# Kernel optimization log

Hardware: AMD Instinct MI355X
Metric: run time of the kernel (lower is better)

Reference implementation:

```python
import jax, jax.numpy as jnp
import numpy as np

B, T, I, H = 8192, 2048, 2, 20


def setup_inputs() -> dict:
    key = jax.random.key(0)
    ks = jax.random.split(key, 7)
    s = 1.0 / np.sqrt(H).astype(np.float32)  # PyTorch RNN/Linear init bound
    u = lambda k, shp: jax.random.uniform(k, shp, minval=-s, maxval=s, dtype=jnp.float32)
    return {
        "x": jax.random.normal(ks[0], (B, T, I), dtype=jnp.float32),
        "W_ih": u(ks[1], (H, I)),
        "W_hh": u(ks[2], (H, H)),
        "b_ih": u(ks[3], (H,)),
        "b_hh": u(ks[4], (H,)),
        "fc_w": u(ks[5], (1, H)),
        "fc_b": u(ks[6], (1,)),
    }


def reference(x, W_ih, W_hh, b_ih, b_hh, fc_w, fc_b):
    # x: [B, T, I] (batch_first). Precompute input contribution for all steps.
    # xw: [T, B, H] -- time-major for lax.scan
    xw = jnp.einsum("bti,hi->tbh", x, W_ih) + b_ih + b_hh
    h0 = jnp.zeros((x.shape[0], H), dtype=x.dtype)

    def step(h, xw_t):
        h_new = jnp.tanh(xw_t + h @ W_hh.T)  # tanh-RNN recurrence
        return h_new, None

    hT, _ = jax.lax.scan(step, h0, xw)
    out = hT @ fc_w.T + fc_b          # fc on last timestep: [B, 1]
    h_state = hT[None]                # [1, B, H] like nn.RNN's h_n
    return out, h_state
```

## Files before the change

### kernel.cpp

```cpp
#include <hip/hip_runtime.h>


#define T_STEPS 2048
#define B_ROWS  8192
#define NCHUNK  (T_STEPS / 8)

#define XOR1_CTRL 0xB1
#define XOR2_CTRL 0x4E
#define MIR7_CTRL 0x141

#define ROW_F 28

typedef float f32x2 __attribute__((ext_vector_type(2)));

__device__ __forceinline__ float tanh_fast(float a) {
    float e = __builtin_amdgcn_exp2f(a * 2.8853900817779268f);
    float r = __builtin_amdgcn_rcpf(e + 1.0f);
    return fmaf(-2.0f, r, 1.0f);
}

template <int CTRL>
__device__ __forceinline__ float dpp_full(float v) {
    return __int_as_float(__builtin_amdgcn_update_dpp(
        0, __float_as_int(v), CTRL, 0xF, 0xF, true));
}

__device__ __forceinline__ void pk_fma_acc(f32x2& c, f32x2 a, f32x2 b) {
    asm("v_pk_fma_f32 %0, %1, %2, %0" : "+v"(c) : "v"(a), "v"(b));
}
__device__ __forceinline__ f32x2 pk_fma3(f32x2 a, f32x2 b, f32x2 c) {
    f32x2 d;
    asm("v_pk_fma_f32 %0, %1, %2, %3" : "=v"(d) : "v"(a), "v"(b), "v"(c));
    return d;
}

__global__ __launch_bounds__(64, 1) void rnn_fused(
    const float* __restrict__ x,
    const float* __restrict__ W_ih,
    const float* __restrict__ W_hh,
    const float* __restrict__ b_ih,
    const float* __restrict__ b_hh,
    const float* __restrict__ fc_w,
    const float* __restrict__ fc_b,
    float* __restrict__ out)
{
    const int lane = threadIdx.x & 63;
    const int g    = lane & 7;
    const int r    = lane >> 3;
    const int row  = blockIdx.x * 8 + r;

    __shared__ float hsm[8 * ROW_F];

    f32x2 W2[3][12];
    f32x2 wiP[3], bP[3];
    float fcw[3];
#pragma unroll
    for (int jj = 0; jj < 3; ++jj) {
        const int j = 3 * g + jj;
        const bool v = (j < 20);
#pragma unroll
        for (int p = 0; p < 12; ++p) {
            const int k0 = 2 * p, k1 = 2 * p + 1;
            W2[jj][p].x = (v && k0 < 20) ? W_hh[j * 20 + k0] : 0.0f;
            W2[jj][p].y = (v && k1 < 20) ? W_hh[j * 20 + k1] : 0.0f;
        }
        wiP[jj].x = v ? W_ih[j * 2 + 0] : 0.0f;
        wiP[jj].y = v ? W_ih[j * 2 + 1] : 0.0f;
        bP[jj].x  = v ? (b_ih[j] + b_hh[j]) : 0.0f;
        bP[jj].y  = 0.0f;
        fcw[jj]   = v ? fc_w[j] : 0.0f;
    }

    float*       hw   = &hsm[r * ROW_F + 3 * g];
    const float4* hr4 = (const float4*)&hsm[r * ROW_F];

    float h0 = 0.0f, h1 = 0.0f, h2 = 0.0f;
    float4 hq[6];

    hw[0] = 0.0f; hw[1] = 0.0f; hw[2] = 0.0f;
#pragma unroll
    for (int i = 0; i < 6; ++i) hq[i] = hr4[i];

    auto step = [&](float x0, float x1) {
        f32x2 xp; xp.x = x0; xp.y = x1;
        f32x2 c0 = pk_fma3(xp, wiP[0], bP[0]);
        f32x2 c1 = pk_fma3(xp, wiP[1], bP[1]);
        f32x2 c2 = pk_fma3(xp, wiP[2], bP[2]);
        const f32x2* hp = (const f32x2*)hq;
#pragma unroll
        for (int p = 0; p < 12; ++p) {
            pk_fma_acc(c0, hp[p], W2[0][p]);
            pk_fma_acc(c1, hp[p], W2[1][p]);
            pk_fma_acc(c2, hp[p], W2[2][p]);
        }
        h0 = tanh_fast(c0.x + c0.y);
        h1 = tanh_fast(c1.x + c1.y);
        h2 = tanh_fast(c2.x + c2.y);
        hw[0] = h0; hw[1] = h1; hw[2] = h2;
#pragma unroll
        for (int i = 0; i < 6; ++i) hq[i] = hr4[i];
    };

    const float4* xq = (const float4*)(x + (size_t)row * (T_STEPS * 2));
    float4 q[4], qn[4];
#pragma unroll
    for (int i = 0; i < 4; ++i) q[i] = xq[i];

#pragma unroll 1
    for (int c = 0; c < NCHUNK; c += 2) {
        const int c1 = c + 1;
        const int c2 = (c + 2 < NCHUNK) ? (c + 2) : c1;
#pragma unroll
        for (int i = 0; i < 4; ++i) qn[i] = xq[4 * c1 + i];

        step(q[0].x, q[0].y); step(q[0].z, q[0].w);
        step(q[1].x, q[1].y); step(q[1].z, q[1].w);
        step(q[2].x, q[2].y); step(q[2].z, q[2].w);
        step(q[3].x, q[3].y); step(q[3].z, q[3].w);

#pragma unroll
        for (int i = 0; i < 4; ++i) q[i] = xq[4 * c2 + i];

        step(qn[0].x, qn[0].y); step(qn[0].z, qn[0].w);
        step(qn[1].x, qn[1].y); step(qn[1].z, qn[1].w);
        step(qn[2].x, qn[2].y); step(qn[2].z, qn[2].w);
        step(qn[3].x, qn[3].y); step(qn[3].z, qn[3].w);
    }

    {
        const int j0 = 3 * g;
        float* hs = out + B_ROWS + (size_t)row * 20;
        if (j0 + 0 < 20) hs[j0 + 0] = h0;
        if (j0 + 1 < 20) hs[j0 + 1] = h1;
        if (j0 + 2 < 20) hs[j0 + 2] = h2;
    }
    {
        float p = h0 * fcw[0];
        p = fmaf(h1, fcw[1], p);
        p = fmaf(h2, fcw[2], p);
        p += dpp_full<XOR1_CTRL>(p);
        p += dpp_full<XOR2_CTRL>(p);
        p += dpp_full<MIR7_CTRL>(p);
        if (g == 0) out[row] = p + fc_b[0];
    }
}

extern "C" void kernel_launch(void* const* d_in, const int* in_sizes, int n_in,
                              void* d_out, int out_size, void* d_ws, size_t ws_size,
                              hipStream_t stream) {
    const float* x    = (const float*)d_in[0];
    const float* W_ih = (const float*)d_in[1];
    const float* W_hh = (const float*)d_in[2];
    const float* b_ih = (const float*)d_in[3];
    const float* b_hh = (const float*)d_in[4];
    const float* fc_w = (const float*)d_in[5];
    const float* fc_b = (const float*)d_in[6];
    float* out = (float*)d_out;

    rnn_fused<<<1024, 64, 0, stream>>>(x, W_ih, W_hh, b_ih, b_hh, fc_w, fc_b, out);
}
```

Baseline: 568.4 us.

## Exchange half of hidden state via DPP lane shuffles instead of LDS reads

Each lane now gets 12 of the 24 hidden values it needs from its own lane, its mirrored lane and its xor-1 neighbour through DPP moves. The other 12 come from two smaller LDS reads instead of six float4 reads of the whole row, and W_hh columns are permuted per lane to match this order. The goal is less LDS traffic and latency on the serial recurrence path, at the cost of extra DPP instructions and a more intricate index mapping.

New measurement: 533.8 us. 6.1% less time.

```diff
diff --git a/kernel.cpp b/kernel.cpp
--- a/kernel.cpp
+++ b/kernel.cpp
@@ -9,14 +9,18 @@
 #define XOR2_CTRL 0x4E
 #define MIR7_CTRL 0x141
 
-#define ROW_F 28
-
 typedef float f32x2 __attribute__((ext_vector_type(2)));
 
 __device__ __forceinline__ float tanh_fast(float a) {
     float e = __builtin_amdgcn_exp2f(a * 2.8853900817779268f);
     float r = __builtin_amdgcn_rcpf(e + 1.0f);
     return fmaf(-2.0f, r, 1.0f);
+}
+
+template <int CTRL>
+__device__ __forceinline__ float dpp_t(float old_, float src) {
+    return __int_as_float(__builtin_amdgcn_update_dpp(
+        __float_as_int(old_), __float_as_int(src), CTRL, 0xF, 0xF, false));
 }
 
 template <int CTRL>
@@ -49,7 +53,24 @@
     const int r    = lane >> 3;
     const int row  = blockIdx.x * 8 + r;
 
-    __shared__ float hsm[8 * ROW_F];
+    __shared__ float hsm[8 * 24];
+
+    const bool setA = (g == 0) || (g == 1) || (g == 6) || (g == 7);
+
+    int kOf[24];
+    kOf[0]  = 3 * g;        kOf[1]  = 3 * g + 1;
+    kOf[2]  = 3 * g + 2;    kOf[3]  = 3 * (g ^ 7);
+    kOf[4]  = 3 * (g ^ 7) + 1; kOf[5] = 3 * (g ^ 7) + 2;
+    kOf[6]  = 3 * (g ^ 1);  kOf[7]  = 3 * (g ^ 1) + 1;
+    kOf[8]  = 3 * (g ^ 1) + 2; kOf[9] = 3 * (g ^ 6);
+    kOf[10] = 3 * (g ^ 6) + 1; kOf[11] = 3 * (g ^ 6) + 2;
+    const int fb1 = setA ? 6 : 18;
+    const int fb2 = setA ? 12 : 0;
+#pragma unroll
+    for (int i = 0; i < 6; ++i) {
+        kOf[12 + i] = fb1 + i;
+        kOf[18 + i] = fb2 + i;
+    }
 
     f32x2 W2[3][12];
     f32x2 wiP[3], bP[3];
@@ -60,7 +81,7 @@
         const bool v = (j < 20);
 #pragma unroll
         for (int p = 0; p < 12; ++p) {
-            const int k0 = 2 * p, k1 = 2 * p + 1;
+            const int k0 = kOf[2 * p], k1 = kOf[2 * p + 1];
             W2[jj][p].x = (v && k0 < 20) ? W_hh[j * 20 + k0] : 0.0f;
             W2[jj][p].y = (v && k1 < 20) ? W_hh[j * 20 + k1] : 0.0f;
         }
@@ -71,34 +92,48 @@
         fcw[jj]   = v ? fc_w[j] : 0.0f;
     }
 
-    float*       hw   = &hsm[r * ROW_F + 3 * g];
-    const float4* hr4 = (const float4*)&hsm[r * ROW_F];
+    float*       hw  = &hsm[r * 24 + 3 * g];
+    const f32x2* fr1 = (const f32x2*)&hsm[r * 24 + fb1];
+    const f32x2* fr2 = (const f32x2*)&hsm[r * 24 + fb2];
 
-    float h0 = 0.0f, h1 = 0.0f, h2 = 0.0f;
-    float4 hq[6];
-
+    f32x2 n0, n1, n2, n3, n4, n5, f[6];
+    n0 = 0.0f; n1 = 0.0f; n2 = 0.0f; n3 = 0.0f; n4 = 0.0f; n5 = 0.0f;
+#pragma unroll
+    for (int i = 0; i < 6; ++i) f[i] = 0.0f;
     hw[0] = 0.0f; hw[1] = 0.0f; hw[2] = 0.0f;
-#pragma unroll
-    for (int i = 0; i < 6; ++i) hq[i] = hr4[i];
 
     auto step = [&](float x0, float x1) {
+        n1.y = dpp_t<MIR7_CTRL>(n1.y, n0.x);
+        n2.x = dpp_t<MIR7_CTRL>(n2.x, n0.y);
+        n2.y = dpp_t<MIR7_CTRL>(n2.y, n1.x);
         f32x2 xp; xp.x = x0; xp.y = x1;
         f32x2 c0 = pk_fma3(xp, wiP[0], bP[0]);
         f32x2 c1 = pk_fma3(xp, wiP[1], bP[1]);
         f32x2 c2 = pk_fma3(xp, wiP[2], bP[2]);
-        const f32x2* hp = (const f32x2*)hq;
+        n3.x = dpp_t<XOR1_CTRL>(n3.x, n0.x);
+        n3.y = dpp_t<XOR1_CTRL>(n3.y, n0.y);
+        n4.x = dpp_t<XOR1_CTRL>(n4.x, n1.x);
+        n4.y = dpp_t<XOR1_CTRL>(n4.y, n1.y);
+        n5.x = dpp_t<XOR1_CTRL>(n5.x, n2.x);
+        n5.y = dpp_t<XOR1_CTRL>(n5.y, n2.y);
+        pk_fma_acc(c0, n0, W2[0][0]); pk_fma_acc(c1, n0, W2[1][0]); pk_fma_acc(c2, n0, W2[2][0]);
+        pk_fma_acc(c0, n1, W2[0][1]); pk_fma_acc(c1, n1, W2[1][1]); pk_fma_acc(c2, n1, W2[2][1]);
+        pk_fma_acc(c0, n2, W2[0][2]); pk_fma_acc(c1, n2, W2[1][2]); pk_fma_acc(c2, n2, W2[2][2]);
+        pk_fma_acc(c0, n3, W2[0][3]); pk_fma_acc(c1, n3, W2[1][3]); pk_fma_acc(c2, n3, W2[2][3]);
+        pk_fma_acc(c0, n4, W2[0][4]); pk_fma_acc(c1, n4, W2[1][4]); pk_fma_acc(c2, n4, W2[2][4]);
+        pk_fma_acc(c0, n5, W2[0][5]); pk_fma_acc(c1, n5, W2[1][5]); pk_fma_acc(c2, n5, W2[2][5]);
 #pragma unroll
-        for (int p = 0; p < 12; ++p) {
-            pk_fma_acc(c0, hp[p], W2[0][p]);
-            pk_fma_acc(c1, hp[p], W2[1][p]);
-            pk_fma_acc(c2, hp[p], W2[2][p]);
+        for (int i = 0; i < 6; ++i) {
+            pk_fma_acc(c0, f[i], W2[0][6 + i]);
+            pk_fma_acc(c1, f[i], W2[1][6 + i]);
+            pk_fma_acc(c2, f[i], W2[2][6 + i]);
         }
-        h0 = tanh_fast(c0.x + c0.y);
-        h1 = tanh_fast(c1.x + c1.y);
-        h2 = tanh_fast(c2.x + c2.y);
-        hw[0] = h0; hw[1] = h1; hw[2] = h2;
-#pragma unroll
-        for (int i = 0; i < 6; ++i) hq[i] = hr4[i];
+        n0.x = tanh_fast(c0.x + c0.y);
+        n0.y = tanh_fast(c1.x + c1.y);
+        n1.x = tanh_fast(c2.x + c2.y);
+        hw[0] = n0.x; hw[1] = n0.y; hw[2] = n1.x;
+        f[0] = fr1[0]; f[1] = fr1[1]; f[2] = fr1[2];
+        f[3] = fr2[0]; f[4] = fr2[1]; f[5] = fr2[2];
     };
 
     const float4* xq = (const float4*)(x + (size_t)row * (T_STEPS * 2));
@@ -130,14 +165,14 @@
     {
         const int j0 = 3 * g;
         float* hs = out + B_ROWS + (size_t)row * 20;
-        if (j0 + 0 < 20) hs[j0 + 0] = h0;
-        if (j0 + 1 < 20) hs[j0 + 1] = h1;
-        if (j0 + 2 < 20) hs[j0 + 2] = h2;
+        if (j0 + 0 < 20) hs[j0 + 0] = n0.x;
+        if (j0 + 1 < 20) hs[j0 + 1] = n0.y;
+        if (j0 + 2 < 20) hs[j0 + 2] = n1.x;
     }
     {
-        float p = h0 * fcw[0];
-        p = fmaf(h1, fcw[1], p);
-        p = fmaf(h2, fcw[2], p);
+        float p = n0.x * fcw[0];
+        p = fmaf(n0.y, fcw[1], p);
+        p = fmaf(n1.x, fcw[2], p);
         p += dpp_full<XOR1_CTRL>(p);
         p += dpp_full<XOR2_CTRL>(p);
         p += dpp_full<MIR7_CTRL>(p);
```
